# Kernel optimization log

Hardware: AMD Instinct MI355X
Metric: run time of the kernel (lower is better)

Reference implementation:

```python
import jax, jax.numpy as jnp
import numpy as np

C = 128; HEADS = 8; GH = 32; GW = 32; B = 8; PD = 8  # PD = (dim//4)//4

def _conv(x, w, pad, dil=1, groups=1):
    return jax.lax.conv_general_dilated(
        x, w, (1, 1), [(pad[0], pad[0]), (pad[1], pad[1])],
        rhs_dilation=(dil, dil),
        dimension_numbers=('NCHW', 'OIHW', 'NCHW'),
        feature_group_count=groups)

def _lrelu(t):
    return jnp.where(t >= 0, t, 0.1 * t)

def _ln(t, g, b, eps=1e-5):
    m = jnp.mean(t, -1, keepdims=True)
    v = jnp.var(t, -1, keepdims=True)
    return (t - m) * jax.lax.rsqrt(v + eps) * g + b

def setup_inputs():
    rng = np.random.RandomState(0)
    f = lambda *s: jnp.asarray((rng.randn(*s) * 0.05).astype(np.float32))
    ones = lambda n: jnp.ones((n,), jnp.float32)
    zeros = lambda n: jnp.zeros((n,), jnp.float32)
    # Swin-style relative position index over the (GH, GW) group
    coords = np.stack(np.meshgrid(np.arange(GH), np.arange(GW), indexing='ij')).reshape(2, -1)
    rel = (coords[:, :, None] - coords[:, None, :]).transpose(1, 2, 0)
    rel[..., 0] += GH - 1; rel[..., 1] += GW - 1; rel[..., 0] *= 2 * GW - 1
    rel_idx = jnp.asarray(rel.sum(-1).astype(np.int32))  # [N, N]
    biases = np.stack(np.meshgrid(np.arange(1 - GH, GH), np.arange(1 - GW, GW), indexing='ij'))
    biases = jnp.asarray(biases.reshape(2, -1).T.astype(np.float32))  # [(2GH-1)*(2GW-1), 2]
    return dict(
        x=jnp.asarray(rng.rand(B, C, GH, GW).astype(np.float32)),
        conv1_w=f(C, C, 3, 3), conv2_w=f(C, C, 3, 3), conv3_w=f(C, C, 3, 3),
        convt_w=f(C, 3, 1, 1),
        rba_w=f(C, C, 3, 1), rba_b=zeros(C), rbb_w=f(C, C, 1, 3), rbb_b=zeros(C),
        pp_w=f(PD, 2), pp_b=zeros(PD),
        l1_g=ones(PD), l1_b=zeros(PD), l1_w=f(PD, PD), l1_b2=zeros(PD),
        l2_g=ones(PD), l2_b=zeros(PD), l2_w=f(PD, PD), l2_b2=zeros(PD),
        l3_g=ones(PD), l3_b=zeros(PD), l3_w=f(HEADS, PD), l3_b2=zeros(HEADS),
        qk_w=f(2 * C, C), qk_b=zeros(2 * C),
        v_w=f(C, C), v_b=zeros(C),
        proj_w=f(C, C), proj_b=zeros(C),
        fc1_w=f(C, C), fc1_b=zeros(C), fc2_w=f(C, C), fc2_b=zeros(C),
        biases=biases, rel_idx=rel_idx,
    )

def reference(x, conv1_w, conv2_w, conv3_w, convt_w, rba_w, rba_b, rbb_w, rbb_b,
              pp_w, pp_b, l1_g, l1_b, l1_w, l1_b2, l2_g, l2_b, l2_w, l2_b2,
              l3_g, l3_b, l3_w, l3_b2, qk_w, qk_b, v_w, v_b, proj_w, proj_b,
              fc1_w, fc1_b, fc2_w, fc2_b, biases, rel_idx):
    Bn, Cc, Hh, Ww = x.shape
    N = Hh * Ww
    hd = Cc // HEADS
    # FeaExtract: ResASPP (3 dilated 3x3 convs, grouped 1x1 merge) + residual
    b1 = _lrelu(_conv(x, conv1_w, (1, 1)))
    b2 = _lrelu(_conv(x, conv2_w, (3, 3), dil=3))
    b3 = _lrelu(_conv(x, conv3_w, (5, 5), dil=5))
    a = _conv(jnp.concatenate([b1, b2, b3], 1), convt_w, (0, 0), groups=Cc) + x
    # RB: (3,1) conv -> lrelu -> (1,3) conv + residual
    r = _lrelu(_conv(a, rba_w, (1, 0)) + rba_b[None, :, None, None])
    r = _conv(r, rbb_w, (0, 1)) + rbb_b[None, :, None, None]
    o0 = r + a
    # original uses in-place clamp_, so o0 is clamped before flattening
    o0 = jnp.clip(o0, 0.0, 1.0)
    E = o0.reshape(Bn, Cc, N).transpose(0, 2, 1)  # [B, N, C]
    qk = E @ qk_w.T + qk_b  # [B, N, 2C]
    q = qk[..., :Cc].reshape(Bn, N, HEADS, hd).transpose(0, 2, 1, 3)
    k = qk[..., Cc:].reshape(Bn, N, HEADS, hd).transpose(0, 2, 1, 3)
    v = (E @ v_w.T + v_b).reshape(Bn, N, HEADS, hd).transpose(0, 2, 1, 3)
    attn = jnp.einsum('bhid,bhjd->bhij', q * (hd ** -0.5), k)
    # DynamicPosBias MLP (residual=False): Linear(2,pd) -> [LN,ReLU,Linear] x2 -> LN,ReLU,Linear(pd,heads)
    p = biases @ pp_w.T + pp_b
    p = jax.nn.relu(_ln(p, l1_g, l1_b)) @ l1_w.T + l1_b2
    p = jax.nn.relu(_ln(p, l2_g, l2_b)) @ l2_w.T + l2_b2
    p = jax.nn.relu(_ln(p, l3_g, l3_b)) @ l3_w.T + l3_b2  # [L, heads]
    rpb = p[rel_idx]  # gather -> [N, N, heads]
    attn = attn + rpb.transpose(2, 0, 1)[None]
    attn = jax.nn.softmax(attn, axis=-1)
    y = jnp.einsum('bhij,bhjd->bhid', attn, v).transpose(0, 2, 1, 3).reshape(Bn, N, Cc) + E
    x_proj = y @ proj_w.T + proj_b
    h = jax.nn.gelu(x_proj @ fc1_w.T + fc1_b, approximate=False)
    return (h @ fc2_w.T + fc2_b) + y
```

## Files before the change

### kernel.cpp

```cpp
#include <hip/hip_runtime.h>
#include <hip/hip_bf16.h>

typedef __hip_bfloat16 bf16;
typedef __bf16 bf16x8 __attribute__((ext_vector_type(8)));
typedef float f32x4 __attribute__((ext_vector_type(4)));
typedef __fp16 f16x2 __attribute__((ext_vector_type(2)));
typedef __fp16 f16x4 __attribute__((ext_vector_type(4)));

#define Lb 3969
#define LOG2E 1.4426950408889634f
#define EXP2(x) __builtin_amdgcn_exp2f(x)

#define XP_F   0
#define WF_F   903168
#define WR_F   1124352
#define WG_F   1173504
#define BH_F   1222656
#define R1P_F  1222656
#define QKV_F  1222656
#define AP_F   2795520
#define YT_F   2795520
#define EB_F   3352576
#define RPB_F  3876864
#define FLAG_F 3908616
#define RT_F   3908624
#define VT_F   4924432

__device__ __forceinline__ float b2f(bf16 v) { return __bfloat162float(v); }
__device__ __forceinline__ bf16 f2b(float v) { return __float2bfloat16(v); }

template <typename T> __device__ __forceinline__ float ldw(const void* p, int i);
template <> __device__ __forceinline__ float ldw<bf16>(const void* p, int i) {
  return __bfloat162float(((const bf16*)p)[i]);
}
template <> __device__ __forceinline__ float ldw<float>(const void* p, int i) {
  return ((const float*)p)[i];
}
template <typename T> __device__ __forceinline__ void stw(void* p, size_t i, float v);
template <> __device__ __forceinline__ void stw<bf16>(void* p, size_t i, float v) {
  ((bf16*)p)[i] = __float2bfloat16(v);
}
template <> __device__ __forceinline__ void stw<float>(void* p, size_t i, float v) {
  ((float*)p)[i] = v;
}

__device__ __forceinline__ unsigned pkh(float a, float b) {
  f16x2 t = __builtin_amdgcn_cvt_pkrtz(a, b);
  return *(unsigned*)&t;
}

__device__ __forceinline__ bool detect_local(const unsigned* x) {
  int lane = threadIdx.x & 63;
  int cnt = 0;
#pragma unroll
  for (int k = 0; k < 4; ++k) {
    unsigned lo = x[lane + 64 * k] & 0xFFFFu;
    cnt += (lo >= 0x3C00u && lo < 0x3F80u) ? 1 : 0;
  }
#pragma unroll
  for (int off = 1; off < 64; off <<= 1) cnt += __shfl_xor(cnt, off);
  return cnt >= 128;
}

template <typename T>
__device__ void wprep_all_body(const void* w1, const void* w2, const void* w3,
                               const void* rba_w, const void* rbb_w,
                               const void* qk_w, const void* v_w,
                               const void* proj_w, const void* fc1_w,
                               const void* fc2_w, bf16* __restrict__ Wf,
                               bf16* __restrict__ Wr, bf16* __restrict__ Wg)
{
  int tid = blockIdx.x * 256 + threadIdx.x;
  int lane = tid & 63, li = lane & 15, quad = lane >> 4;
  if (tid < 55296) {
    int mt = (tid >> 6) & 7;
    int Kc = (tid >> 9) & 3;
    int rem = tid >> 11;
    int t = rem % 9;
    int br = rem / 9;
    const void* w = (br == 0 ? w1 : (br == 1 ? w2 : w3));
    int o = mt * 16 + li;
    int ci0 = Kc * 32 + quad * 8;
#pragma unroll
    for (int j = 0; j < 8; ++j)
      Wf[(size_t)tid * 8 + j] = f2b(ldw<T>(w, (o * 128 + ci0 + j) * 9 + t));
  } else {
    int u = tid - 55296;
    if (u < 12288) {
      int Kc = (u >> 6) & 3, mt = (u >> 8) & 7, q = u >> 11;
      const void* w = (q >= 3) ? rbb_w : rba_w;
      int t = q % 3;
#pragma unroll
      for (int j = 0; j < 8; ++j)
        Wr[(size_t)u * 8 + j] =
            f2b(ldw<T>(w, ((mt * 16 + li) * 128 + Kc * 32 + quad * 8 + j) * 3 + t));
    } else if (u < 24576) {
      int g = u - 12288;
      int Kc = (g >> 6) & 3, mtg = g >> 8;
      const void* w; int mrow; float sc = 1.f;
      if (mtg < 16)      { w = qk_w;   mrow = mtg * 16;
                           if (mtg < 8) sc = 0.25f * LOG2E; }
      else if (mtg < 24) { w = v_w;    mrow = (mtg - 16) * 16; }
      else if (mtg < 32) { w = proj_w; mrow = (mtg - 24) * 16; }
      else if (mtg < 40) { w = fc1_w;  mrow = (mtg - 32) * 16; }
      else               { w = fc2_w;  mrow = (mtg - 40) * 16; }
#pragma unroll
      for (int j = 0; j < 8; ++j)
        Wg[(size_t)g * 8 + j] =
            f2b(sc * ldw<T>(w, (mrow + li) * 128 + Kc * 32 + quad * 8 + j));
    }
  }
}

template <typename T>
__device__ void nhwc_body(const void* x, bf16* __restrict__ xp,
                          bf16 (*tile)[128], int bid)
{
  const int b = bid >> 5;
  const int row = bid & 31;
  const int t = threadIdx.x;
  const size_t bbase = (size_t)b * 42 * 42 * 128;
  const bf16x8 z = (bf16x8){};

  if (t < 160) {
    int side = t / 80;
    int off = (t % 80) * 8;
    *(bf16x8*)&xp[bbase + ((size_t)(row + 5) * 42 + side * 37) * 128 + off] = z;
  }
  {
    int zr = (row < 5) ? row : ((row >= 27) ? row + 10 : -1);
    if (zr >= 0) {
      size_t base = bbase + (size_t)zr * 42 * 128;
      for (int k = t; k < 672; k += 256) *(bf16x8*)&xp[base + k * 8] = z;
    }
  }

  {
    int ci = t >> 1, half = t & 1;
#pragma unroll
    for (int j = 0; j < 16; ++j) {
      int px = half * 16 + j;
      tile[px][ci] = f2b(ldw<T>(x, ((size_t)b * 128 + ci) * 1024 + row * 32 + px));
    }
  }
  __syncthreads();
  {
    int px = t >> 3, c0 = (t & 7) * 16;
    bf16* dst = xp + (bbase + ((size_t)(row + 5) * 42 + (px + 5)) * 128 + c0);
#pragma unroll
    for (int j = 0; j < 16; ++j) dst[j] = tile[px][c0 + j];
  }
}

__global__ __launch_bounds__(256) void prep_kernel(
    const unsigned* x, const void* w1, const void* w2, const void* w3,
    const void* rba_w, const void* rbb_w, const void* qk_w, const void* v_w,
    const void* proj_w, const void* fc1_w, const void* fc2_w,
    bf16* Wf, bf16* Wr, bf16* Wg, bf16* xp, int* flag)
{
  __shared__ bf16 tile[32][128];
  bool isbf = detect_local(x);
  if (blockIdx.x < 312) {
    if (blockIdx.x == 0 && threadIdx.x == 0) *flag = isbf ? 1 : 0;
    if (isbf) wprep_all_body<bf16>(w1, w2, w3, rba_w, rbb_w, qk_w, v_w, proj_w,
                                   fc1_w, fc2_w, Wf, Wr, Wg);
    else      wprep_all_body<float>(w1, w2, w3, rba_w, rbb_w, qk_w, v_w, proj_w,
                                    fc1_w, fc2_w, Wf, Wr, Wg);
  } else {
    int bid = blockIdx.x - 312;
    if (isbf) nhwc_body<bf16>(x, xp, tile, bid);
    else      nhwc_body<float>(x, xp, tile, bid);
  }
}

__global__ __launch_bounds__(256) void aspp2_kernel(
    const bf16* __restrict__ xp, const bf16* __restrict__ Wf,
    bf16* __restrict__ bh)
{
  const int nt_ = blockIdx.x, br = blockIdx.y >> 1, mh = blockIdx.y & 1;
  const int bb = blockIdx.z;
  const int w = threadIdx.x >> 6, lane = threadIdx.x & 63;
  const int quad = lane >> 4, li = lane & 15;
  const int d = (br == 0 ? 1 : (br == 1 ? 3 : 5));
  const int pxw = nt_ * 64 + w * 16;
  const int y = pxw >> 5, xb = pxw & 31;

  f32x4 acc[4] = {};
  const bf16* Wbase = Wf + (size_t)br * 18432 * 8 + (size_t)mh * 4 * 64 * 8;

  for (int t = 0; t < 9; ++t) {
    const int dy = (t / 3 - 1) * d, dx = (t % 3 - 1) * d;
    const bf16* Asite =
        xp + (((size_t)bb * 42 + (y + 5 + dy)) * 42 + (xb + li + 5 + dx)) * 128;
    const bf16* Wt = Wbase + (size_t)t * 2048 * 8;
#pragma unroll
    for (int Kc = 0; Kc < 4; ++Kc) {
      bf16x8 afrag = *(const bf16x8*)(Asite + Kc * 32 + quad * 8);
      const bf16* Wk = Wt + (size_t)Kc * 512 * 8 + (size_t)lane * 8;
#pragma unroll
      for (int mt = 0; mt < 4; ++mt) {
        bf16x8 wfrag = *(const bf16x8*)(Wk + (size_t)mt * 64 * 8);
        acc[mt] = __builtin_amdgcn_mfma_f32_16x16x32_bf16(afrag, wfrag, acc[mt],
                                                          0, 0, 0);
      }
    }
  }
#pragma unroll
  for (int mt = 0; mt < 4; ++mt)
#pragma unroll
    for (int r = 0; r < 4; ++r) {
      int px = pxw + quad * 4 + r;
      bh[((size_t)bb * 1024 + px) * 384 + br * 128 + (mh * 4 + mt) * 16 + li] =
          f2b(acc[mt][r]);
    }
}

template <typename T>
__device__ void merge2_body(const bf16* __restrict__ xp, const void* wt,
                            const bf16* __restrict__ bh, bf16* __restrict__ ap,
                            float* cw)
{
  const int b = blockIdx.y, px0 = blockIdx.x * 32;
  const bf16x8 z = (bf16x8){};
  if (blockIdx.x == 0) {
    size_t base = ((size_t)b * 34 + 0) * 32 * 128;
    for (int k = threadIdx.x; k < 512; k += 256) *(bf16x8*)&ap[base + k * 8] = z;
  } else if (blockIdx.x == 31) {
    size_t base = ((size_t)b * 34 + 33) * 32 * 128;
    for (int k = threadIdx.x; k < 512; k += 256) *(bf16x8*)&ap[base + k * 8] = z;
  }
  for (int i = threadIdx.x; i < 384; i += 256) cw[i] = ldw<T>(wt, i);
  __syncthreads();
  const int pxl = threadIdx.x >> 3, og = threadIdx.x & 7;
  const int px = px0 + pxl, o0 = og * 16;
  const int y = px >> 5, x = px & 31;
  const bf16* brow = bh + ((size_t)b * 1024 + px) * 384 + o0 * 3;
  const bf16* xrow = xp + (((size_t)b * 42 + y + 5) * 42 + x + 5) * 128 + o0;
  bf16* arow = ap + (((size_t)b * 34 + y + 1) * 32 + x) * 128 + o0;

  bf16 bl[48], xl[16], ol[16];
#pragma unroll
  for (int k = 0; k < 6; ++k) *(bf16x8*)&bl[k * 8] = *(const bf16x8*)&brow[k * 8];
  *(bf16x8*)&xl[0] = *(const bf16x8*)&xrow[0];
  *(bf16x8*)&xl[8] = *(const bf16x8*)&xrow[8];
#pragma unroll
  for (int j = 0; j < 16; ++j) {
    float v = b2f(xl[j]);
#pragma unroll
    for (int i = 0; i < 3; ++i) {
      float t = b2f(bl[j * 3 + i]);
      v += cw[(o0 + j) * 3 + i] * (t >= 0.f ? t : 0.1f * t);
    }
    ol[j] = f2b(v);
  }
  *(bf16x8*)&arow[0] = *(bf16x8*)&ol[0];
  *(bf16x8*)&arow[8] = *(bf16x8*)&ol[8];
}

__global__ __launch_bounds__(256) void merge2_kernel(
    const bf16* xp, const void* wt, const bf16* bh, bf16* ap, const int* flag)
{
  __shared__ float cw[384];
  if (*flag) merge2_body<bf16>(xp, wt, bh, ap, cw);
  else       merge2_body<float>(xp, wt, bh, ap, cw);
}

template <typename T>
__device__ void rb1_body(const bf16* __restrict__ ap, const bf16* __restrict__ Wr,
                         const void* bias, bf16* __restrict__ r1p)
{
  const int b = blockIdx.z, mh = blockIdx.y;
  const int lane = threadIdx.x;
  const int quad = lane >> 4, li = lane & 15;
  const int pxw = blockIdx.x * 16;
  const int y = pxw >> 5, xb = pxw & 31;
  f32x4 acc[4] = {};
#pragma unroll
  for (int t = 0; t < 3; ++t) {
    const bf16* Asite = ap + (((size_t)b * 34 + y + t) * 32 + xb + li) * 128;
#pragma unroll
    for (int Kc = 0; Kc < 4; ++Kc) {
      bf16x8 afrag = *(const bf16x8*)(Asite + Kc * 32 + quad * 8);
#pragma unroll
      for (int mt = 0; mt < 4; ++mt) {
        int f = (t * 8 + mh * 4 + mt) * 4 + Kc;
        bf16x8 wfrag = *(const bf16x8*)(Wr + ((size_t)f * 64 + lane) * 8);
        acc[mt] = __builtin_amdgcn_mfma_f32_16x16x32_bf16(afrag, wfrag, acc[mt],
                                                          0, 0, 0);
      }
    }
  }
  if (quad == 0) {
    int xcol = (xb == 0) ? 0 : 33;
#pragma unroll
    for (int mt = 0; mt < 4; ++mt)
      r1p[(((size_t)b * 32 + y) * 34 + xcol) * 128 + (mh * 4 + mt) * 16 + li] =
          f2b(0.f);
  }
#pragma unroll
  for (int mt = 0; mt < 4; ++mt) {
    int o = (mh * 4 + mt) * 16 + li;
    float bv = ldw<T>(bias, o);
#pragma unroll
    for (int r = 0; r < 4; ++r) {
      int x = xb + quad * 4 + r;
      float v = acc[mt][r] + bv;
      v = (v >= 0.f ? v : 0.1f * v);
      r1p[(((size_t)b * 32 + y) * 34 + x + 1) * 128 + o] = f2b(v);
    }
  }
}

__global__ __launch_bounds__(64) void rb1_kernel(
    const bf16* ap, const bf16* Wr, const void* bias, bf16* r1p, const int* flag)
{
  if (*flag) rb1_body<bf16>(ap, Wr, bias, r1p);
  else       rb1_body<float>(ap, Wr, bias, r1p);
}

template <typename T>
__device__ void rb2_body(const bf16* __restrict__ r1p, const bf16* __restrict__ Wr,
                         const void* bias, const bf16* __restrict__ ap,
                         bf16* __restrict__ Eb)
{
  const int b = blockIdx.z, mh = blockIdx.y;
  const int lane = threadIdx.x;
  const int quad = lane >> 4, li = lane & 15;
  const int pxw = blockIdx.x * 16;
  const int y = pxw >> 5, xb = pxw & 31;
  f32x4 acc[4] = {};
#pragma unroll
  for (int t = 0; t < 3; ++t) {
    const bf16* Asite = r1p + (((size_t)b * 32 + y) * 34 + xb + li + t) * 128;
#pragma unroll
    for (int Kc = 0; Kc < 4; ++Kc) {
      bf16x8 afrag = *(const bf16x8*)(Asite + Kc * 32 + quad * 8);
#pragma unroll
      for (int mt = 0; mt < 4; ++mt) {
        int f = ((3 + t) * 8 + mh * 4 + mt) * 4 + Kc;
        bf16x8 wfrag = *(const bf16x8*)(Wr + ((size_t)f * 64 + lane) * 8);
        acc[mt] = __builtin_amdgcn_mfma_f32_16x16x32_bf16(afrag, wfrag, acc[mt],
                                                          0, 0, 0);
      }
    }
  }
#pragma unroll
  for (int mt = 0; mt < 4; ++mt) {
    int o = (mh * 4 + mt) * 16 + li;
    float bv = ldw<T>(bias, o);
#pragma unroll
    for (int r = 0; r < 4; ++r) {
      int x = xb + quad * 4 + r;
      float v = acc[mt][r] + bv +
                b2f(ap[(((size_t)b * 34 + y + 1) * 32 + x) * 128 + o]);
      v = fminf(fmaxf(v, 0.f), 1.f);
      Eb[((size_t)b * 1024 + y * 32 + x) * 128 + o] = f2b(v);
    }
  }
}

__global__ __launch_bounds__(64) void rb2_kernel(
    const bf16* r1p, const bf16* Wr, const void* bias, const bf16* ap,
    bf16* Eb, const int* flag)
{
  if (*flag) rb2_body<bf16>(r1p, Wr, bias, ap, Eb);
  else       rb2_body<float>(r1p, Wr, bias, ap, Eb);
}

template <typename T>
__device__ __forceinline__ void ln_relu8(const float* t, float* u,
                                         const void* g, const void* bb)
{
  float m = 0.f;
#pragma unroll
  for (int k = 0; k < 8; ++k) m += t[k];
  m *= 0.125f;
  float v = 0.f;
#pragma unroll
  for (int k = 0; k < 8; ++k) { float d = t[k] - m; v += d * d; }
  v *= 0.125f;
  float r = rsqrtf(v + 1e-5f);
#pragma unroll
  for (int k = 0; k < 8; ++k) {
    float val = (t[k] - m) * r * ldw<T>(g, k) + ldw<T>(bb, k);
    u[k] = val > 0.f ? val : 0.f;
  }
}

template <typename T>
__device__ void dpb_body(const void* biases, const void* pp_w, const void* pp_b,
                         const void* l1_g, const void* l1_b, const void* l1_w,
                         const void* l1_b2, const void* l2_g, const void* l2_b,
                         const void* l2_w, const void* l2_b2, const void* l3_g,
                         const void* l3_b, const void* l3_w, const void* l3_b2,
                         float* __restrict__ RPB)
{
  int r = blockIdx.x * 256 + threadIdx.x;
  if (r >= Lb) return;
  float b0 = ldw<T>(biases, r * 2), b1 = ldw<T>(biases, r * 2 + 1);
  float t[8], u[8];
#pragma unroll
  for (int j = 0; j < 8; ++j)
    t[j] = b0 * ldw<T>(pp_w, j * 2) + b1 * ldw<T>(pp_w, j * 2 + 1) +
           ldw<T>(pp_b, j);
  ln_relu8<T>(t, u, l1_g, l1_b);
#pragma unroll
  for (int j = 0; j < 8; ++j) {
    float s = ldw<T>(l1_b2, j);
#pragma unroll
    for (int k = 0; k < 8; ++k) s += u[k] * ldw<T>(l1_w, j * 8 + k);
    t[j] = s;
  }
  ln_relu8<T>(t, u, l2_g, l2_b);
#pragma unroll
  for (int j = 0; j < 8; ++j) {
    float s = ldw<T>(l2_b2, j);
#pragma unroll
    for (int k = 0; k < 8; ++k) s += u[k] * ldw<T>(l2_w, j * 8 + k);
    t[j] = s;
  }
  ln_relu8<T>(t, u, l3_g, l3_b);
#pragma unroll
  for (int h = 0; h < 8; ++h) {
    float s = ldw<T>(l3_b2, h);
#pragma unroll
    for (int k = 0; k < 8; ++k) s += u[k] * ldw<T>(l3_w, h * 8 + k);
    RPB[h * Lb + r] = s;
  }
}

__global__ __launch_bounds__(256) void dpb_kernel(
    const void* biases, const void* pp_w, const void* pp_b, const void* l1_g,
    const void* l1_b, const void* l1_w, const void* l1_b2, const void* l2_g,
    const void* l2_b, const void* l2_w, const void* l2_b2, const void* l3_g,
    const void* l3_b, const void* l3_w, const void* l3_b2, float* RPB,
    const int* flag)
{
  if (*flag)
    dpb_body<bf16>(biases, pp_w, pp_b, l1_g, l1_b, l1_w, l1_b2, l2_g, l2_b,
                   l2_w, l2_b2, l3_g, l3_b, l3_w, l3_b2, RPB);
  else
    dpb_body<float>(biases, pp_w, pp_b, l1_g, l1_b, l1_w, l1_b2, l2_g, l2_b,
                    l2_w, l2_b2, l3_g, l3_b, l3_w, l3_b2, RPB);
}

__global__ __launch_bounds__(64) void rt_kernel(
    const float* __restrict__ RPB, float* __restrict__ RTf)
{
  const int tt = blockIdx.x, h = blockIdx.y;
  const int t = tt >> 1, p = tt & 1;
  const int lane = threadIdx.x, quad = lane >> 4, li = lane & 15;
  const float* rp = RPB + h * Lb;
  float* dst = RTf + ((size_t)(h * 124 + tt) * 4) * 256 + lane * 4;
#pragma unroll
  for (int mt = 0; mt < 4; ++mt) {
    f32x4 v;
#pragma unroll
    for (int r = 0; r < 4; ++r) {
      int j = mt * 16 + quad * 4 + r;
      int dy = (t - 30) - (j >> 5);
      int dx = (p * 16 + li) - (j & 31);
      v[r] = rp[(dy + 31) * 63 + dx + 31] * LOG2E;
    }
    *(f32x4*)(dst + mt * 256) = v;
  }
}

template <typename T>
__device__ void qkv_body(const bf16* __restrict__ Eb, const bf16* __restrict__ Wg,
                         const void* qk_b, const void* v_b,
                         bf16* __restrict__ QKV, uint2* __restrict__ VTh)
{
  const int grp = blockIdx.y, b = blockIdx.z;
  const int w = threadIdx.x >> 6, lane = threadIdx.x & 63;
  const int quad = lane >> 4, li = lane & 15;
  const int pxw = blockIdx.x * 64 + w * 16;
  bf16x8 ef[4];
#pragma unroll
  for (int Kc = 0; Kc < 4; ++Kc)
    ef[Kc] = *(const bf16x8*)&Eb[((size_t)b * 1024 + pxw + li) * 128 + Kc * 32 +
                                 quad * 8];
  f32x4 acc[8] = {};
#pragma unroll
  for (int nt = 0; nt < 8; ++nt) {
    int g = grp * 8 + nt;
#pragma unroll
    for (int Kc = 0; Kc < 4; ++Kc) {
      bf16x8 wf = *(const bf16x8*)&Wg[(((size_t)g * 4 + Kc) * 64 + lane) * 8];
      acc[nt] = __builtin_amdgcn_mfma_f32_16x16x32_bf16(ef[Kc], wf, acc[nt],
                                                        0, 0, 0);
    }
  }
  if (grp < 2) {
#pragma unroll
    for (int nt = 0; nt < 8; ++nt) {
      int g = grp * 8 + nt;
      int o = g * 16 + li;
      float bv = (g < 8) ? (0.25f * LOG2E) * ldw<T>(qk_b, o) : ldw<T>(qk_b, o);
#pragma unroll
      for (int r = 0; r < 4; ++r) {
        int px = pxw + quad * 4 + r;
        QKV[((size_t)b * 1024 + px) * 384 + o] = f2b(acc[nt][r] + bv);
      }
    }
  } else {
#pragma unroll
    for (int nt = 0; nt < 8; ++nt) {
      int hh = nt;
      float bv = ldw<T>(v_b, nt * 16 + li);
      uint2 pu;
      pu.x = pkh(acc[nt][0] + bv, acc[nt][1] + bv);
      pu.y = pkh(acc[nt][2] + bv, acc[nt][3] + bv);
      VTh[(((size_t)(b * 8 + hh) * 16 + blockIdx.x) * 4 + w) * 64 + lane] = pu;
    }
  }
}

__global__ __launch_bounds__(256) void qkv_kernel(
    const bf16* Eb, const bf16* Wg, const void* qk_b, const void* v_b,
    bf16* QKV, uint2* VTh, const int* flag)
{
  if (*flag) qkv_body<bf16>(Eb, Wg, qk_b, v_b, QKV, VTh);
  else       qkv_body<float>(Eb, Wg, qk_b, v_b, QKV, VTh);
}

template <typename T>
__device__ void mlpf_body(const bf16* __restrict__ Yt, const bf16* __restrict__ Wg,
                          const void* proj_b, const void* fc1_b,
                          const void* fc2_b, void* out,
                          bf16 (*buf0)[136], bf16 (*buf1)[136])
{
  const int w = threadIdx.x >> 6, lane = threadIdx.x & 63;
  const int quad = lane >> 4, li = lane & 15;
  const size_t row0 = (size_t)blockIdx.x * 16;

  bf16x8 ef[4];
  f32x4 acc[2];

#pragma unroll
  for (int Kc = 0; Kc < 4; ++Kc)
    ef[Kc] = *(const bf16x8*)&Yt[(row0 + li) * 128 + Kc * 32 + quad * 8];
  acc[0] = (f32x4){}; acc[1] = (f32x4){};
#pragma unroll
  for (int j = 0; j < 2; ++j) {
    int g = 24 + w * 2 + j;
#pragma unroll
    for (int Kc = 0; Kc < 4; ++Kc) {
      bf16x8 wf = *(const bf16x8*)&Wg[(((size_t)g * 4 + Kc) * 64 + lane) * 8];
      acc[j] = __builtin_amdgcn_mfma_f32_16x16x32_bf16(ef[Kc], wf, acc[j],
                                                       0, 0, 0);
    }
  }
#pragma unroll
  for (int j = 0; j < 2; ++j) {
    int o = (w * 2 + j) * 16 + li;
    float bv = ldw<T>(proj_b, o);
#pragma unroll
    for (int r = 0; r < 4; ++r)
      buf0[quad * 4 + r][o] = f2b(acc[j][r] + bv);
  }
  __syncthreads();

#pragma unroll
  for (int Kc = 0; Kc < 4; ++Kc)
    ef[Kc] = *(const bf16x8*)&buf0[li][Kc * 32 + quad * 8];
  acc[0] = (f32x4){}; acc[1] = (f32x4){};
#pragma unroll
  for (int j = 0; j < 2; ++j) {
    int g = 32 + w * 2 + j;
#pragma unroll
    for (int Kc = 0; Kc < 4; ++Kc) {
      bf16x8 wf = *(const bf16x8*)&Wg[(((size_t)g * 4 + Kc) * 64 + lane) * 8];
      acc[j] = __builtin_amdgcn_mfma_f32_16x16x32_bf16(ef[Kc], wf, acc[j],
                                                       0, 0, 0);
    }
  }
#pragma unroll
  for (int j = 0; j < 2; ++j) {
    int o = (w * 2 + j) * 16 + li;
    float bv = ldw<T>(fc1_b, o);
#pragma unroll
    for (int r = 0; r < 4; ++r) {
      float v = acc[j][r] + bv;
      v = 0.5f * v * (1.f + erff(v * 0.70710678118f));
      buf1[quad * 4 + r][o] = f2b(v);
    }
  }
  __syncthreads();

#pragma unroll
  for (int Kc = 0; Kc < 4; ++Kc)
    ef[Kc] = *(const bf16x8*)&buf1[li][Kc * 32 + quad * 8];
  acc[0] = (f32x4){}; acc[1] = (f32x4){};
#pragma unroll
  for (int j = 0; j < 2; ++j) {
    int g = 40 + w * 2 + j;
#pragma unroll
    for (int Kc = 0; Kc < 4; ++Kc) {
      bf16x8 wf = *(const bf16x8*)&Wg[(((size_t)g * 4 + Kc) * 64 + lane) * 8];
      acc[j] = __builtin_amdgcn_mfma_f32_16x16x32_bf16(ef[Kc], wf, acc[j],
                                                       0, 0, 0);
    }
  }
#pragma unroll
  for (int j = 0; j < 2; ++j) {
    int o = (w * 2 + j) * 16 + li;
    float bv = ldw<T>(fc2_b, o);
#pragma unroll
    for (int r = 0; r < 4; ++r) {
      size_t oidx = (row0 + quad * 4 + r) * 128 + o;
      float v = acc[j][r] + bv + b2f(Yt[oidx]);
      stw<T>(out, oidx, v);
    }
  }
}

__global__ __launch_bounds__(256) void mlpf_kernel(
    const bf16* Yt, const bf16* Wg, const void* proj_b, const void* fc1_b,
    const void* fc2_b, void* out, const int* flag)
{
  __shared__ bf16 buf0[16][136];
  __shared__ bf16 buf1[16][136];
  if (*flag) mlpf_body<bf16>(Yt, Wg, proj_b, fc1_b, fc2_b, out, buf0, buf1);
  else       mlpf_body<float>(Yt, Wg, proj_b, fc1_b, fc2_b, out, buf0, buf1);
}

__global__ __launch_bounds__(256, 4) void attn_kernel(
    const bf16* __restrict__ QKV, const bf16* __restrict__ Eb,
    const float* __restrict__ RTf, const uint2* __restrict__ VTh,
    bf16* __restrict__ Yt)
{
  const int qt = blockIdx.x * 4 + (threadIdx.x >> 6);
  const int hh = blockIdx.y;
  const int b = blockIdx.z;

  const int lane = threadIdx.x & 63;
  const int quad = lane >> 4, li = lane & 15;
  const int qb = qt * 16;

  const bf16* QKVb = QKV + (size_t)b * 1024 * 384;
  const uint2* VTb = VTh + (size_t)(b * 8 + hh) * 4096;
  const float* RTh = RTf + (size_t)hh * 124 * 1024;

  bf16x8 qf = (bf16x8){};
  if (quad < 2)
    qf = *(const bf16x8*)&QKVb[(size_t)(qb + li) * 384 + hh * 16 + quad * 8];

  f32x4 Oa = {}, Ob = {};
  float m_st = -1e30f, l_ln = 0.f;
  const int sbase = (lane & 48) + ((lane >> 2) & 12);

  struct Buf { bf16x8 kf[4]; f32x4 cin[4]; uint2 vb[4]; };
  Buf bA, bB;

  auto LOAD = [&](Buf& bf, int c) {
    const int c0 = c * 64;
    const int tt = ((qt >> 1) - 2 * c + 30) * 2 + (qt & 1);
    const float* rtp = RTh + (size_t)tt * 1024 + lane * 4;
#pragma unroll
    for (int mt = 0; mt < 4; ++mt) {
      bf.cin[mt] = *(const f32x4*)(rtp + mt * 256);
      bf.kf[mt] = (bf16x8){};
      if (quad < 2)
        bf.kf[mt] = *(const bf16x8*)&QKVb[(size_t)(c0 + mt * 16 + li) * 384 +
                                          128 + hh * 16 + quad * 8];
      bf.vb[mt] = VTb[(size_t)(c * 4 + mt) * 64 + lane];
    }
  };

  auto STEP = [&](const Buf& bf) {
    f32x4 sT[4];
#pragma unroll
    for (int mt = 0; mt < 4; ++mt)
      sT[mt] = __builtin_amdgcn_mfma_f32_16x16x32_bf16(bf.kf[mt], qf,
                                                       bf.cin[mt], 0, 0, 0);

    float m0 = fmaxf(fmaxf(sT[0][0], sT[0][1]), fmaxf(sT[0][2], sT[0][3]));
    float m1 = fmaxf(fmaxf(sT[1][0], sT[1][1]), fmaxf(sT[1][2], sT[1][3]));
    float m2 = fmaxf(fmaxf(sT[2][0], sT[2][1]), fmaxf(sT[2][2], sT[2][3]));
    float m3 = fmaxf(fmaxf(sT[3][0], sT[3][1]), fmaxf(sT[3][2], sT[3][3]));
    float lmax = fmaxf(fmaxf(m0, m1), fmaxf(m2, m3));

    if (!__all(lmax <= m_st + 11.5f)) {
      float cm = fmaxf(lmax, __shfl_xor(lmax, 16));
      cm = fmaxf(cm, __shfl_xor(cm, 32));
      float mn = fmaxf(m_st, cm);
      float al = EXP2(m_st - mn);
      m_st = mn;
      l_ln *= al;
#pragma unroll
      for (int r = 0; r < 4; ++r) {
        float a = __shfl(al, sbase + r);
        Oa[r] *= a;
        Ob[r] *= a;
      }
    }

#pragma unroll
    for (int mt = 0; mt < 4; ++mt)
#pragma unroll
      for (int r = 0; r < 4; ++r) sT[mt][r] = EXP2(sT[mt][r] - m_st);

    float s0 = (sT[0][0] + sT[0][1]) + (sT[0][2] + sT[0][3]);
    float s1 = (sT[1][0] + sT[1][1]) + (sT[1][2] + sT[1][3]);
    float s2 = (sT[2][0] + sT[2][1]) + (sT[2][2] + sT[2][3]);
    float s3 = (sT[3][0] + sT[3][1]) + (sT[3][2] + sT[3][3]);
    l_ln += (s0 + s1) + (s2 + s3);

#pragma unroll
    for (int mt = 0; mt < 4; ++mt) {
      union { unsigned u[2]; f16x4 h4; } pu;
      pu.u[0] = pkh(sT[mt][0], sT[mt][1]);
      pu.u[1] = pkh(sT[mt][2], sT[mt][3]);
      union { uint2 u; f16x4 h; } vu;
      vu.u = bf.vb[mt];
      if (mt & 2)
        Ob = __builtin_amdgcn_mfma_f32_16x16x16f16(pu.h4, vu.h, Ob, 0, 0, 0);
      else
        Oa = __builtin_amdgcn_mfma_f32_16x16x16f16(pu.h4, vu.h, Oa, 0, 0, 0);
    }
  };

  LOAD(bA, 0);
  for (int c = 0; c < 16; c += 2) {
    LOAD(bB, c + 1);
    STEP(bA);
    if (c + 2 < 16) LOAD(bA, c + 2);
    STEP(bB);
  }

  float l_st = l_ln + __shfl_xor(l_ln, 16);
  l_st += __shfl_xor(l_st, 32);

  f32x4 O_;
#pragma unroll
  for (int r = 0; r < 4; ++r) O_[r] = Oa[r] + Ob[r];

  const bf16* Ebp = Eb + (size_t)b * 1024 * 128 + hh * 16 + li;
  bf16* Ytp = Yt + (size_t)b * 1024 * 128 + hh * 16 + li;
#pragma unroll
  for (int r = 0; r < 4; ++r) {
    float lb = __shfl(l_st, sbase + r);
    int qrow = qb + quad * 4 + r;
    Ytp[(size_t)qrow * 128] =
        f2b(O_[r] / lb + b2f(Ebp[(size_t)qrow * 128]));
  }
}

extern "C" void kernel_launch(void* const* d_in, const int* in_sizes, int n_in,
                              void* d_out, int out_size, void* d_ws,
                              size_t ws_size, hipStream_t stream)
{
  (void)in_sizes; (void)n_in; (void)out_size; (void)ws_size;
  const void* x       = d_in[0];
  const void* conv1_w = d_in[1];
  const void* conv2_w = d_in[2];
  const void* conv3_w = d_in[3];
  const void* convt_w = d_in[4];
  const void* rba_w   = d_in[5];
  const void* rba_b   = d_in[6];
  const void* rbb_w   = d_in[7];
  const void* rbb_b   = d_in[8];
  const void* pp_w    = d_in[9];
  const void* pp_b    = d_in[10];
  const void* l1_g    = d_in[11];
  const void* l1_b    = d_in[12];
  const void* l1_w    = d_in[13];
  const void* l1_b2   = d_in[14];
  const void* l2_g    = d_in[15];
  const void* l2_b    = d_in[16];
  const void* l2_w    = d_in[17];
  const void* l2_b2   = d_in[18];
  const void* l3_g    = d_in[19];
  const void* l3_b    = d_in[20];
  const void* l3_w    = d_in[21];
  const void* l3_b2   = d_in[22];
  const void* qk_w    = d_in[23];
  const void* qk_b    = d_in[24];
  const void* v_w     = d_in[25];
  const void* v_b     = d_in[26];
  const void* proj_w  = d_in[27];
  const void* proj_b  = d_in[28];
  const void* fc1_w   = d_in[29];
  const void* fc1_b   = d_in[30];
  const void* fc2_w   = d_in[31];
  const void* fc2_b   = d_in[32];
  const void* biases  = d_in[33];

  float* ws   = (float*)d_ws;
  bf16*  xp   = (bf16*)(ws + XP_F);
  bf16*  Wf   = (bf16*)(ws + WF_F);
  bf16*  Wr   = (bf16*)(ws + WR_F);
  bf16*  Wg   = (bf16*)(ws + WG_F);
  bf16*  bh   = (bf16*)(ws + BH_F);
  bf16*  r1p  = (bf16*)(ws + R1P_F);
  bf16*  QKV  = (bf16*)(ws + QKV_F);
  bf16*  ap   = (bf16*)(ws + AP_F);
  bf16*  Yt   = (bf16*)(ws + YT_F);
  bf16*  Eb   = (bf16*)(ws + EB_F);
  float* RPB  = ws + RPB_F;
  int*   flag = (int*)(ws + FLAG_F);
  float* RTf  = ws + RT_F;
  uint2* VTh  = (uint2*)(ws + VT_F);

  prep_kernel<<<568, 256, 0, stream>>>(
      (const unsigned*)x, conv1_w, conv2_w, conv3_w, rba_w, rbb_w, qk_w, v_w,
      proj_w, fc1_w, fc2_w, Wf, Wr, Wg, xp, flag);
  aspp2_kernel<<<dim3(16, 6, 8), 256, 0, stream>>>(xp, Wf, bh);
  merge2_kernel<<<dim3(32, 8), 256, 0, stream>>>(xp, convt_w, bh, ap, flag);
  rb1_kernel<<<dim3(64, 2, 8), 64, 0, stream>>>(ap, Wr, rba_b, r1p, flag);
  rb2_kernel<<<dim3(64, 2, 8), 64, 0, stream>>>(r1p, Wr, rbb_b, ap, Eb, flag);
  dpb_kernel<<<16, 256, 0, stream>>>(biases, pp_w, pp_b, l1_g, l1_b, l1_w,
                                     l1_b2, l2_g, l2_b, l2_w, l2_b2, l3_g,
                                     l3_b, l3_w, l3_b2, RPB, flag);
  rt_kernel<<<dim3(124, 8), 64, 0, stream>>>(RPB, RTf);
  qkv_kernel<<<dim3(16, 3, 8), 256, 0, stream>>>(Eb, Wg, qk_b, v_b, QKV, VTh,
                                                 flag);
  attn_kernel<<<dim3(16, 8, 8), 256, 0, stream>>>(QKV, Eb, RTf, VTh, Yt);
  mlpf_kernel<<<512, 256, 0, stream>>>(Yt, Wg, proj_b, fc1_b, fc2_b, d_out,
                                       flag);
}
```

Measured before the change: 233.0 us.

## Fuse residual-block convs via shared-memory row and fuse DPB MLP into bias tiling

```diff
diff --git a/kernel.cpp b/kernel.cpp
--- a/kernel.cpp
+++ b/kernel.cpp
@@ -16,7 +16,6 @@
 #define WR_F   1124352
 #define WG_F   1173504
 #define BH_F   1222656
-#define R1P_F  1222656
 #define QKV_F  1222656
 #define AP_F   2795520
 #define YT_F   2795520
@@ -266,14 +265,20 @@
 }
 
 template <typename T>
-__device__ void rb1_body(const bf16* __restrict__ ap, const bf16* __restrict__ Wr,
-                         const void* bias, bf16* __restrict__ r1p)
-{
-  const int b = blockIdx.z, mh = blockIdx.y;
-  const int lane = threadIdx.x;
+__device__ void rbf_body(const bf16* __restrict__ ap, const bf16* __restrict__ Wr,
+                         const void* rba_b, const void* rbb_b,
+                         bf16* __restrict__ Eb, bf16 (*r1row)[136])
+{
+  const int y = blockIdx.x, b = blockIdx.y;
+  const int w = threadIdx.x >> 6, lane = threadIdx.x & 63;
+  const int mh = w & 1, xb = (w >> 1) * 16;
   const int quad = lane >> 4, li = lane & 15;
-  const int pxw = blockIdx.x * 16;
-  const int y = pxw >> 5, xb = pxw & 31;
+
+  if (threadIdx.x < 128) {
+    r1row[0][threadIdx.x] = f2b(0.f);
+    r1row[33][threadIdx.x] = f2b(0.f);
+  }
+
   f32x4 acc[4] = {};
 #pragma unroll
   for (int t = 0; t < 3; ++t) {
@@ -290,68 +295,42 @@
       }
     }
   }
-  if (quad == 0) {
-    int xcol = (xb == 0) ? 0 : 33;
-#pragma unroll
-    for (int mt = 0; mt < 4; ++mt)
-      r1p[(((size_t)b * 32 + y) * 34 + xcol) * 128 + (mh * 4 + mt) * 16 + li] =
-          f2b(0.f);
-  }
 #pragma unroll
   for (int mt = 0; mt < 4; ++mt) {
     int o = (mh * 4 + mt) * 16 + li;
-    float bv = ldw<T>(bias, o);
+    float bv = ldw<T>(rba_b, o);
 #pragma unroll
     for (int r = 0; r < 4; ++r) {
       int x = xb + quad * 4 + r;
       float v = acc[mt][r] + bv;
-      v = (v >= 0.f ? v : 0.1f * v);
-      r1p[(((size_t)b * 32 + y) * 34 + x + 1) * 128 + o] = f2b(v);
-    }
-  }
-}
-
-__global__ __launch_bounds__(64) void rb1_kernel(
-    const bf16* ap, const bf16* Wr, const void* bias, bf16* r1p, const int* flag)
-{
-  if (*flag) rb1_body<bf16>(ap, Wr, bias, r1p);
-  else       rb1_body<float>(ap, Wr, bias, r1p);
-}
-
-template <typename T>
-__device__ void rb2_body(const bf16* __restrict__ r1p, const bf16* __restrict__ Wr,
-                         const void* bias, const bf16* __restrict__ ap,
-                         bf16* __restrict__ Eb)
-{
-  const int b = blockIdx.z, mh = blockIdx.y;
-  const int lane = threadIdx.x;
-  const int quad = lane >> 4, li = lane & 15;
-  const int pxw = blockIdx.x * 16;
-  const int y = pxw >> 5, xb = pxw & 31;
-  f32x4 acc[4] = {};
+      r1row[x + 1][o] = f2b(v >= 0.f ? v : 0.1f * v);
+    }
+  }
+  __syncthreads();
+
+  f32x4 acc2[4] = {};
 #pragma unroll
   for (int t = 0; t < 3; ++t) {
-    const bf16* Asite = r1p + (((size_t)b * 32 + y) * 34 + xb + li + t) * 128;
 #pragma unroll
     for (int Kc = 0; Kc < 4; ++Kc) {
-      bf16x8 afrag = *(const bf16x8*)(Asite + Kc * 32 + quad * 8);
+      bf16x8 afrag = *(const bf16x8*)&r1row[xb + li + t][Kc * 32 + quad * 8];
 #pragma unroll
       for (int mt = 0; mt < 4; ++mt) {
         int f = ((3 + t) * 8 + mh * 4 + mt) * 4 + Kc;
         bf16x8 wfrag = *(const bf16x8*)(Wr + ((size_t)f * 64 + lane) * 8);
-        acc[mt] = __builtin_amdgcn_mfma_f32_16x16x32_bf16(afrag, wfrag, acc[mt],
-                                                          0, 0, 0);
+        acc2[mt] = __builtin_amdgcn_mfma_f32_16x16x32_bf16(afrag, wfrag,
+                                                           acc2[mt], 0, 0, 0);
       }
     }
   }
 #pragma unroll
   for (int mt = 0; mt < 4; ++mt) {
     int o = (mh * 4 + mt) * 16 + li;
-    float bv = ldw<T>(bias, o);
+    float bv = ldw<T>(rbb_b, o);
 #pragma unroll
     for (int r = 0; r < 4; ++r) {
       int x = xb + quad * 4 + r;
-      float v = acc[mt][r] + bv +
+      float v = acc2[mt][r] + bv +
                 b2f(ap[(((size_t)b * 34 + y + 1) * 32 + x) * 128 + o]);
       v = fminf(fmaxf(v, 0.f), 1.f);
       Eb[((size_t)b * 1024 + y * 32 + x) * 128 + o] = f2b(v);
@@ -359,12 +338,13 @@
   }
 }
 
-__global__ __launch_bounds__(64) void rb2_kernel(
-    const bf16* r1p, const bf16* Wr, const void* bias, const bf16* ap,
+__global__ __launch_bounds__(256) void rbf_kernel(
+    const bf16* ap, const bf16* Wr, const void* rba_b, const void* rbb_b,
     bf16* Eb, const int* flag)
 {
-  if (*flag) rb2_body<bf16>(r1p, Wr, bias, ap, Eb);
-  else       rb2_body<float>(r1p, Wr, bias, ap, Eb);
+  __shared__ bf16 r1row[34][136];
+  if (*flag) rbf_body<bf16>(ap, Wr, rba_b, rbb_b, Eb, r1row);
+  else       rbf_body<float>(ap, Wr, rba_b, rbb_b, Eb, r1row);
 }
 
 template <typename T>
@@ -388,15 +368,12 @@
 }
 
 template <typename T>
-__device__ void dpb_body(const void* biases, const void* pp_w, const void* pp_b,
-                         const void* l1_g, const void* l1_b, const void* l1_w,
-                         const void* l1_b2, const void* l2_g, const void* l2_b,
-                         const void* l2_w, const void* l2_b2, const void* l3_g,
-                         const void* l3_b, const void* l3_w, const void* l3_b2,
-                         float* __restrict__ RPB)
-{
-  int r = blockIdx.x * 256 + threadIdx.x;
-  if (r >= Lb) return;
+__device__ __forceinline__ float dpb_one(
+    int r, int h, const void* biases, const void* pp_w, const void* pp_b,
+    const void* l1_g, const void* l1_b, const void* l1_w, const void* l1_b2,
+    const void* l2_g, const void* l2_b, const void* l2_w, const void* l2_b2,
+    const void* l3_g, const void* l3_b, const void* l3_w, const void* l3_b2)
+{
   float b0 = ldw<T>(biases, r * 2), b1 = ldw<T>(biases, r * 2 + 1);
   float t[8], u[8];
 #pragma unroll
@@ -420,37 +397,34 @@
     t[j] = s;
   }
   ln_relu8<T>(t, u, l3_g, l3_b);
-#pragma unroll
-  for (int h = 0; h < 8; ++h) {
-    float s = ldw<T>(l3_b2, h);
-#pragma unroll
-    for (int k = 0; k < 8; ++k) s += u[k] * ldw<T>(l3_w, h * 8 + k);
-    RPB[h * Lb + r] = s;
-  }
-}
-
-__global__ __launch_bounds__(256) void dpb_kernel(
+  float s = ldw<T>(l3_b2, h);
+#pragma unroll
+  for (int k = 0; k < 8; ++k) s += u[k] * ldw<T>(l3_w, h * 8 + k);
+  return s;
+}
+
+template <typename T>
+__device__ void dpbrt_body(
     const void* biases, const void* pp_w, const void* pp_b, const void* l1_g,
     const void* l1_b, const void* l1_w, const void* l1_b2, const void* l2_g,
     const void* l2_b, const void* l2_w, const void* l2_b2, const void* l3_g,
-    const void* l3_b, const void* l3_w, const void* l3_b2, float* RPB,
-    const int* flag)
-{
-  if (*flag)
-    dpb_body<bf16>(biases, pp_w, pp_b, l1_g, l1_b, l1_w, l1_b2, l2_g, l2_b,
-                   l2_w, l2_b2, l3_g, l3_b, l3_w, l3_b2, RPB);
-  else
-    dpb_body<float>(biases, pp_w, pp_b, l1_g, l1_b, l1_w, l1_b2, l2_g, l2_b,
-                    l2_w, l2_b2, l3_g, l3_b, l3_w, l3_b2, RPB);
-}
-
-__global__ __launch_bounds__(64) void rt_kernel(
-    const float* __restrict__ RPB, float* __restrict__ RTf)
+    const void* l3_b, const void* l3_w, const void* l3_b2,
+    float* __restrict__ RTf, float (*rpl)[47])
 {
   const int tt = blockIdx.x, h = blockIdx.y;
   const int t = tt >> 1, p = tt & 1;
   const int lane = threadIdx.x, quad = lane >> 4, li = lane & 15;
-  const float* rp = RPB + h * Lb;
+
+  for (int e = lane; e < 94; e += 64) {
+    int row = t + e / 47;
+    int col = p * 16 + e % 47;
+    rpl[e / 47][e % 47] =
+        dpb_one<T>(row * 63 + col, h, biases, pp_w, pp_b, l1_g, l1_b, l1_w,
+                   l1_b2, l2_g, l2_b, l2_w, l2_b2, l3_g, l3_b, l3_w, l3_b2) *
+        LOG2E;
+  }
+  __syncthreads();
+
   float* dst = RTf + ((size_t)(h * 124 + tt) * 4) * 256 + lane * 4;
 #pragma unroll
   for (int mt = 0; mt < 4; ++mt) {
@@ -458,12 +432,26 @@
 #pragma unroll
     for (int r = 0; r < 4; ++r) {
       int j = mt * 16 + quad * 4 + r;
-      int dy = (t - 30) - (j >> 5);
-      int dx = (p * 16 + li) - (j & 31);
-      v[r] = rp[(dy + 31) * 63 + dx + 31] * LOG2E;
+      v[r] = rpl[1 - (j >> 5)][li - (j & 31) + 31];
     }
     *(f32x4*)(dst + mt * 256) = v;
   }
+}
+
+__global__ __launch_bounds__(64) void dpbrt_kernel(
+    const void* biases, const void* pp_w, const void* pp_b, const void* l1_g,
+    const void* l1_b, const void* l1_w, const void* l1_b2, const void* l2_g,
+    const void* l2_b, const void* l2_w, const void* l2_b2, const void* l3_g,
+    const void* l3_b, const void* l3_w, const void* l3_b2, float* RTf,
+    const int* flag)
+{
+  __shared__ float rpl[2][47];
+  if (*flag)
+    dpbrt_body<bf16>(biases, pp_w, pp_b, l1_g, l1_b, l1_w, l1_b2, l2_g, l2_b,
+                     l2_w, l2_b2, l3_g, l3_b, l3_w, l3_b2, RTf, rpl);
+  else
+    dpbrt_body<float>(biases, pp_w, pp_b, l1_g, l1_b, l1_w, l1_b2, l2_g, l2_b,
+                      l2_w, l2_b2, l3_g, l3_b, l3_w, l3_b2, RTf, rpl);
 }
 
 template <typename T>
@@ -793,12 +781,10 @@
   bf16*  Wr   = (bf16*)(ws + WR_F);
   bf16*  Wg   = (bf16*)(ws + WG_F);
   bf16*  bh   = (bf16*)(ws + BH_F);
-  bf16*  r1p  = (bf16*)(ws + R1P_F);
   bf16*  QKV  = (bf16*)(ws + QKV_F);
   bf16*  ap   = (bf16*)(ws + AP_F);
   bf16*  Yt   = (bf16*)(ws + YT_F);
   bf16*  Eb   = (bf16*)(ws + EB_F);
-  float* RPB  = ws + RPB_F;
   int*   flag = (int*)(ws + FLAG_F);
   float* RTf  = ws + RT_F;
   uint2* VTh  = (uint2*)(ws + VT_F);
@@ -808,12 +794,10 @@
       proj_w, fc1_w, fc2_w, Wf, Wr, Wg, xp, flag);
   aspp2_kernel<<<dim3(16, 6, 8), 256, 0, stream>>>(xp, Wf, bh);
   merge2_kernel<<<dim3(32, 8), 256, 0, stream>>>(xp, convt_w, bh, ap, flag);
-  rb1_kernel<<<dim3(64, 2, 8), 64, 0, stream>>>(ap, Wr, rba_b, r1p, flag);
-  rb2_kernel<<<dim3(64, 2, 8), 64, 0, stream>>>(r1p, Wr, rbb_b, ap, Eb, flag);
-  dpb_kernel<<<16, 256, 0, stream>>>(biases, pp_w, pp_b, l1_g, l1_b, l1_w,
-                                     l1_b2, l2_g, l2_b, l2_w, l2_b2, l3_g,
-                                     l3_b, l3_w, l3_b2, RPB, flag);
-  rt_kernel<<<dim3(124, 8), 64, 0, stream>>>(RPB, RTf);
+  rbf_kernel<<<dim3(32, 8), 256, 0, stream>>>(ap, Wr, rba_b, rbb_b, Eb, flag);
+  dpbrt_kernel<<<dim3(124, 8), 64, 0, stream>>>(
+      biases, pp_w, pp_b, l1_g, l1_b, l1_w, l1_b2, l2_g, l2_b, l2_w, l2_b2,
+      l3_g, l3_b, l3_w, l3_b2, RTf, flag);
   qkv_kernel<<<dim3(16, 3, 8), 256, 0, stream>>>(Eb, Wg, qk_b, v_b, QKV, VTh,
                                                  flag);
   attn_kernel<<<dim3(16, 8, 8), 256, 0, stream>>>(QKV, Eb, RTf, VTh, Yt);
```

Measured after the change: 229.3 us. Within noise of the previous version (-1.6%).
